# Optimization experiments

Hardware: AMD Instinct MI355X
Metric: run time of the kernel (lower is better)

The kernel has to match this reference:

```python
import jax, jax.numpy as jnp
import numpy as np

HIDDEN = 2048
HEAD_DIM = 256
N_HEADS = 8
N_KV_HEADS = 2
N_GROUPS = N_HEADS // N_KV_HEADS
EPS = 1e-6
WAVELENGTH = 10000.0
ROPE_SCALE = 1.0
NEG_INF = -1e9


def setup_inputs() -> dict:
    key = jax.random.key(0)
    ks = jax.random.split(key, 8)
    B, S = 2, 2048
    hidden_states = jax.random.normal(ks[0], (B, S, HIDDEN), dtype=jnp.float32)
    # additive causal mask: 0 on/below diagonal, -1e9 above
    causal = jnp.tril(jnp.ones((S, S), dtype=bool))
    attention_mask = jnp.where(causal, 0.0, NEG_INF).astype(jnp.float32)[None, None]
    attention_mask = jnp.broadcast_to(attention_mask, (B, 1, S, S))
    sd = 1.0 / np.sqrt(HIDDEN)
    wq = jax.random.normal(ks[1], (HIDDEN, N_HEADS * HEAD_DIM), dtype=jnp.float32) * sd
    wk = jax.random.normal(ks[2], (HIDDEN, N_KV_HEADS * HEAD_DIM), dtype=jnp.float32) * sd
    wv = jax.random.normal(ks[3], (HIDDEN, N_KV_HEADS * HEAD_DIM), dtype=jnp.float32) * sd
    wo = jax.random.normal(ks[4], (N_HEADS * HEAD_DIM, HIDDEN), dtype=jnp.float32) * (1.0 / np.sqrt(N_HEADS * HEAD_DIM))
    q_scale = 1.0 + 0.02 * jax.random.normal(ks[5], (HEAD_DIM,), dtype=jnp.float32)
    k_scale = 1.0 + 0.02 * jax.random.normal(ks[6], (HEAD_DIM,), dtype=jnp.float32)
    return {"hidden_states": hidden_states, "attention_mask": attention_mask,
            "wq": wq, "wk": wk, "wv": wv, "wo": wo,
            "q_scale": q_scale, "k_scale": k_scale}


def _rms_norm(x, scale=None):
    # Gemma3nRMSNorm: compute in float32, optional scale, cast back
    x32 = x.astype(jnp.float32)
    out = x32 * jax.lax.rsqrt(jnp.mean(x32 * x32, axis=-1, keepdims=True) + EPS)
    if scale is not None:
        out = out * scale.astype(jnp.float32)
    return out.astype(x.dtype)


def _rope(x, start_index=0):
    # x: [B, S, H, D]; keras-hub RotaryEmbedding (half-split rotate)
    S, D = x.shape[1], x.shape[-1]
    inv_freq = 1.0 / (WAVELENGTH ** (jnp.arange(0, D, 2, dtype=jnp.float32) / D))
    pos = (jnp.arange(S, dtype=jnp.float32) + start_index) / ROPE_SCALE
    freq = jnp.einsum("s,f->sf", pos, inv_freq)           # [S, D/2]
    emb = jnp.concatenate([freq, freq], axis=-1)          # [S, D]
    cos = jnp.cos(emb)[None, :, None, :].astype(x.dtype)
    sin = jnp.sin(emb)[None, :, None, :].astype(x.dtype)
    x1, x2 = jnp.split(x, 2, axis=-1)
    rot = jnp.concatenate([-x2, x1], axis=-1)
    return x * cos + rot * sin


def reference(hidden_states, attention_mask, wq, wk, wv, wo, q_scale, k_scale):
    B, S, _ = hidden_states.shape
    q = (hidden_states @ wq).reshape(B, S, N_HEADS, HEAD_DIM)
    k = (hidden_states @ wk).reshape(B, S, N_KV_HEADS, HEAD_DIM)
    v = (hidden_states @ wv).reshape(B, S, N_KV_HEADS, HEAD_DIM)
    q = _rope(_rms_norm(q, q_scale))
    k = _rope(_rms_norm(k, k_scale))
    v = _rms_norm(v)  # with_scale=False
    # GQA: repeat KV heads, then BHSD layout
    k = jnp.repeat(k, N_GROUPS, axis=2)
    v = jnp.repeat(v, N_GROUPS, axis=2)
    q = q.transpose(0, 2, 1, 3)
    k = k.transpose(0, 2, 1, 3)
    v = v.transpose(0, 2, 1, 3)
    scores = jnp.einsum("bhqd,bhkd->bhqk", q, k) / np.sqrt(HEAD_DIM)
    scores = scores + attention_mask.astype(scores.dtype)
    probs = jax.nn.softmax(scores.astype(jnp.float32), axis=-1).astype(hidden_states.dtype)
    out = jnp.einsum("bhqk,bhkd->bhqd", probs, v)
    out = out.transpose(0, 2, 1, 3).reshape(B, S, N_HEADS * HEAD_DIM)
    return out @ wo
```

## Files before the change

### kernel.cpp

```cpp
#include <hip/hip_runtime.h>
#include <cstdint>
#include <cstddef>

#define SEQ   2048
#define BATCH 2
#define NH    8
#define NKV   2
#define DH    256
#define HID   2048
#define MR    (BATCH*SEQ)

typedef _Float16 h8 __attribute__((ext_vector_type(8)));
typedef _Float16 h4 __attribute__((ext_vector_type(4)));
typedef float   f32x4 __attribute__((ext_vector_type(4)));

__device__ __forceinline__ f32x4 mfma16(h8 a, h8 b, f32x4 c) {
  return __builtin_amdgcn_mfma_f32_16x16x32_f16(a, b, c, 0, 0, 0);
}
__device__ __forceinline__ void gload16(const void* g, void* l) {
  __builtin_amdgcn_global_load_lds((__attribute__((address_space(1))) void*)g,
                                   (__attribute__((address_space(3))) void*)l,
                                   16, 0, 0);
}

__global__ __launch_bounds__(256) void cvt_f16(const float* __restrict__ in,
                                               _Float16* __restrict__ out, int n4) {
  const int i = blockIdx.x * 256 + threadIdx.x;
  if (i >= n4) return;
  const float4 v = ((const float4*)in)[i];
  h4 o = { (_Float16)v.x, (_Float16)v.y, (_Float16)v.z, (_Float16)v.w };
  ((h4*)out)[i] = o;
}

__global__ __launch_bounds__(256) void wtrans(const float* __restrict__ in,
                                              _Float16* __restrict__ out,
                                              int N, int K) {
  __shared__ float L[32][33];
  const int n0 = blockIdx.x * 32, k0 = blockIdx.y * 32;
  const int t = threadIdx.x;
  const int r = t >> 3, c4 = (t & 7) * 4;
  const float4 v = *(const float4*)&in[(size_t)(k0 + r) * N + n0 + c4];
  L[r][c4] = v.x; L[r][c4 + 1] = v.y; L[r][c4 + 2] = v.z; L[r][c4 + 3] = v.w;
  __syncthreads();
  h4 o = { (_Float16)L[c4][r], (_Float16)L[c4 + 1][r],
           (_Float16)L[c4 + 2][r], (_Float16)L[c4 + 3][r] };
  *(h4*)&out[(size_t)(n0 + r) * K + k0 + c4] = o;
}

__global__ __launch_bounds__(256) void gemm_f16(const _Float16* __restrict__ A,
                                                const _Float16* __restrict__ Bt,
                                                float* __restrict__ C,
                                                const int N, const int K) {
  __shared__ __align__(16) unsigned char sm[32768];
  const int t = threadIdx.x, w = t >> 6, lane = t & 63;
  const int l15 = lane & 15, l4 = lane >> 4;
  const int wr = w >> 1, wc = w & 1;
  const int m0 = blockIdx.y * 128, n0 = blockIdx.x * 128;
  const int swz = (l15 & 7) << 4;
  const size_t rb = (size_t)K * 2;

  int rS[4], cS[4];
#pragma unroll
  for (int i = 0; i < 4; ++i) {
    const int o = i * 4096 + w * 1024 + lane * 16;
    rS[i] = o >> 7;
    cS[i] = (o & 127) ^ ((rS[i] & 7) << 4);
  }
  const char* Ab = (const char*)A + (size_t)m0 * rb;
  const char* Bb = (const char*)Bt + (size_t)n0 * rb;

  f32x4 acc[4][4] = {};

  for (int k0 = 0; k0 < K; k0 += 64) {
    __syncthreads();
#pragma unroll
    for (int i = 0; i < 4; ++i) {
      gload16(Ab + (size_t)rS[i] * rb + k0 * 2 + cS[i], sm + i * 4096 + w * 1024);
      gload16(Bb + (size_t)rS[i] * rb + k0 * 2 + cS[i], sm + 16384 + i * 4096 + w * 1024);
    }
    __syncthreads();
#pragma unroll
    for (int kk = 0; kk < 2; ++kk) {
      const int ko = (kk * 64 + l4 * 16) ^ swz;
      h8 av[4], bv[4];
#pragma unroll
      for (int f = 0; f < 4; ++f) {
        av[f] = *(const h8*)(sm + (wr * 64 + f * 16 + l15) * 128 + ko);
        bv[f] = *(const h8*)(sm + 16384 + (wc * 64 + f * 16 + l15) * 128 + ko);
      }
#pragma unroll
      for (int i = 0; i < 4; ++i)
#pragma unroll
        for (int j = 0; j < 4; ++j)
          acc[i][j] = mfma16(av[i], bv[j], acc[i][j]);
    }
  }
#pragma unroll
  for (int i = 0; i < 4; ++i)
#pragma unroll
    for (int r = 0; r < 4; ++r) {
      const int row = m0 + wr * 64 + i * 16 + l4 * 4 + r;
      float* Cp = C + (size_t)row * N + n0 + wc * 64 + l15;
#pragma unroll
      for (int j = 0; j < 4; ++j) Cp[j * 16] = acc[i][j][r];
    }
}

__global__ __launch_bounds__(256) void norm_rope_q(const float* __restrict__ Qp,
                                                   _Float16* __restrict__ Qh,
                                                   const float* __restrict__ q_scale) {
  const int idx = blockIdx.x;
  const int t = threadIdx.x;
  const int h = idx & 7;
  const int bs = idx >> 3;
  const int s = bs & (SEQ - 1);
  const int b = bs >> 11;
  const float x = Qp[(size_t)bs * 2048 + h * 256 + t];
  float ss = x * x;
#pragma unroll
  for (int off = 32; off; off >>= 1) ss += __shfl_xor(ss, off);
  __shared__ float red[4];
  if ((t & 63) == 0) red[t >> 6] = ss;
  __syncthreads();
  const float tot = red[0] + red[1] + red[2] + red[3];
  const float inv = rsqrtf(tot * (1.0f / 256.0f) + 1e-6f);
  const float xn = x * inv * q_scale[t];
  __shared__ float rowbuf[256];
  rowbuf[t] = xn;
  __syncthreads();
  const int f = t & 127;
  const float invf = expf(-0.07195578415606391f * (float)f);
  float sn, cs;
  sincosf((float)s * invf, &sn, &cs);
  const float other = rowbuf[t ^ 128];
  const float o = (t < 128) ? (xn * cs - other * sn) : (xn * cs + other * sn);
  Qh[((size_t)(b * NH + h) * SEQ + s) * DH + t] = (_Float16)o;
}

__global__ __launch_bounds__(256) void norm_kv(const float* __restrict__ KVp,
                                               _Float16* __restrict__ Kh,
                                               _Float16* __restrict__ Vh,
                                               const float* __restrict__ k_scale) {
  const int idx = blockIdx.x;
  const int t = threadIdx.x;
  const bool isK = idx < 8192;
  const int i = isK ? idx : idx - 8192;
  const int kv = i & 1;
  const int bs = i >> 1;
  const int s = bs & (SEQ - 1);
  const int b = bs >> 11;
  const int col = (isK ? kv * DH : 512 + kv * DH) + t;
  const float x = KVp[(size_t)bs * 1024 + col];
  float ss = x * x;
#pragma unroll
  for (int off = 32; off; off >>= 1) ss += __shfl_xor(ss, off);
  __shared__ float red[4];
  if ((t & 63) == 0) red[t >> 6] = ss;
  __syncthreads();
  const float tot = red[0] + red[1] + red[2] + red[3];
  const float inv = rsqrtf(tot * (1.0f / 256.0f) + 1e-6f);
  float xn = x * inv;
  const size_t o = ((size_t)(b * NKV + kv) * SEQ + s) * DH + t;
  if (isK) {
    xn *= k_scale[t];
    __shared__ float rowbuf[256];
    rowbuf[t] = xn;
    __syncthreads();
    const int f = t & 127;
    const float invf = expf(-0.07195578415606391f * (float)f);
    float sn, cs;
    sincosf((float)s * invf, &sn, &cs);
    const float other = rowbuf[t ^ 128];
    const float ov = (t < 128) ? (xn * cs - other * sn) : (xn * cs + other * sn);
    Kh[o] = (_Float16)ov;
  } else {
    Vh[o] = (_Float16)xn;
  }
}

__global__ __launch_bounds__(256) void transpose_v(const _Float16* __restrict__ Vh,
                                                   _Float16* __restrict__ Vt) {
  __shared__ _Float16 L[32][36];
  const int s0 = blockIdx.x * 32, d0 = blockIdx.y * 32;
  const size_t base = (size_t)blockIdx.z * SEQ * DH;
  const int t = threadIdx.x;
  const int r = t >> 3, c4 = (t & 7) * 4;
  const h4 v = *(const h4*)&Vh[base + (size_t)(s0 + r) * DH + d0 + c4];
  L[r][c4] = v.x; L[r][c4 + 1] = v.y; L[r][c4 + 2] = v.z; L[r][c4 + 3] = v.w;
  __syncthreads();
  h4 o = { L[c4][r], L[c4 + 1][r], L[c4 + 2][r], L[c4 + 3][r] };
  *(h4*)&Vt[base + (size_t)(d0 + r) * SEQ + s0 + c4] = o;
}

__global__ __launch_bounds__(256) void attn_f16(const _Float16* __restrict__ Qh,
                                                const _Float16* __restrict__ Kh,
                                                const _Float16* __restrict__ Vt,
                                                _Float16* __restrict__ Ah) {
  __shared__ __align__(16) unsigned char sm[65536];
  const int pid = blockIdx.x;
  const int h = blockIdx.y, b = blockIdx.z;
  const int kh = h >> 2;
  const int t = threadIdx.x, w = t >> 6, lane = t & 63;
  const int l15 = lane & 15, l4 = lane >> 4;
  const int swz = (l15 & 7) << 4;

  const char* Qg = (const char*)(Qh + (size_t)(b * NH + h) * SEQ * DH);
  const char* Kg = (const char*)(Kh + (size_t)(b * NKV + kh) * SEQ * DH);
  const char* Vg = (const char*)(Vt + (size_t)(b * NKV + kh) * DH * SEQ);

  for (int half = 0; half < 2; ++half) {
    const int qt = (half == 0) ? pid : 31 - pid;
    const int q0 = qt * 64;

    __syncthreads();
#pragma unroll
    for (int i = 0; i < 8; ++i) {
      const int o = i * 4096 + w * 1024 + lane * 16;
      const int row = o >> 9;
      const int off = (o & 511) ^ ((row & 7) << 4);
      gload16(Qg + (size_t)(q0 + row) * 512 + off, sm + i * 4096 + w * 1024);
    }
    __syncthreads();
    h8 qf[8];
    {
      const int qrow = w * 16 + l15;
#pragma unroll
      for (int dc = 0; dc < 8; ++dc)
        qf[dc] = *(const h8*)(sm + qrow * 512 + ((dc * 64 + l4 * 16) ^ swz));
    }
    f32x4 o_acc[16] = {};
    float mrun[4] = { -3e38f, -3e38f, -3e38f, -3e38f };
    float lrun[4] = { 0.f, 0.f, 0.f, 0.f };

    for (int kt = 0; kt <= qt; ++kt) {
      __syncthreads();
#pragma unroll
      for (int i = 0; i < 8; ++i) {
        const int o = i * 4096 + w * 1024 + lane * 16;
        const int row = o >> 9;
        const int off = (o & 511) ^ ((row & 7) << 4);
        gload16(Kg + (size_t)(kt * 64 + row) * 512 + off, sm + i * 4096 + w * 1024);
        const int d = o >> 7;
        const int voff = (o & 127) ^ ((d & 7) << 4);
        gload16(Vg + (size_t)d * (SEQ * 2) + kt * 128 + voff,
                sm + 32768 + i * 4096 + w * 1024);
      }
      __syncthreads();

      f32x4 sc[4];
#pragma unroll
      for (int fk = 0; fk < 4; ++fk) {
        f32x4 z = {};
        sc[fk] = z;
        const int krow = fk * 16 + l15;
#pragma unroll
        for (int dc = 0; dc < 8; ++dc) {
          h8 kf = *(const h8*)(sm + krow * 512 + ((dc * 64 + l4 * 16) ^ swz));
          sc[fk] = mfma16(qf[dc], kf, sc[fk]);
        }
      }

      float p[4][4], alpha[4], mnew[4];
#pragma unroll
      for (int r = 0; r < 4; ++r) {
        const int qg = q0 + w * 16 + l4 * 4 + r;
        float mx = -3e38f;
#pragma unroll
        for (int fk = 0; fk < 4; ++fk) {
          const int kg = kt * 64 + fk * 16 + l15;
          float sv = sc[fk][r] * 0.0625f;
          sv = (kg <= qg) ? sv : -3e38f;
          p[fk][r] = sv;
          mx = fmaxf(mx, sv);
        }
#pragma unroll
        for (int msk = 1; msk < 16; msk <<= 1) mx = fmaxf(mx, __shfl_xor(mx, msk));
        mnew[r] = fmaxf(mrun[r], mx);
        alpha[r] = __expf(mrun[r] - mnew[r]);
        mrun[r] = mnew[r];
        float ls = 0.f;
#pragma unroll
        for (int fk = 0; fk < 4; ++fk) {
          const float e = __expf(p[fk][r] - mnew[r]);
          p[fk][r] = e;
          ls += e;
        }
#pragma unroll
        for (int msk = 1; msk < 16; msk <<= 1) ls += __shfl_xor(ls, msk);
        lrun[r] = lrun[r] * alpha[r] + ls;
      }
#pragma unroll
      for (int fd = 0; fd < 16; ++fd)
#pragma unroll
        for (int r = 0; r < 4; ++r) o_acc[fd][r] *= alpha[r];

      __syncthreads();

      unsigned char* Pb = sm + w * 2048;
#pragma unroll
      for (int fk = 0; fk < 4; ++fk)
#pragma unroll
        for (int r = 0; r < 4; ++r) {
          const int qrow = l4 * 4 + r, k = fk * 16 + l15;
          *(_Float16*)(Pb + qrow * 128 + ((k * 2) ^ ((qrow & 7) << 4))) =
              (_Float16)p[fk][r];
        }
#pragma unroll
      for (int kk = 0; kk < 2; ++kk) {
        const h8 pa = *(const h8*)(Pb + l15 * 128 + ((kk * 64 + l4 * 16) ^ swz));
#pragma unroll
        for (int fd = 0; fd < 16; ++fd) {
          const int d = fd * 16 + l15;
          h8 vf = *(const h8*)(sm + 32768 + d * 128 + ((kk * 64 + l4 * 16) ^ swz));
          o_acc[fd] = mfma16(pa, vf, o_acc[fd]);
        }
      }
    }

#pragma unroll
    for (int r = 0; r < 4; ++r) {
      const float linv = 1.0f / lrun[r];
      const int srow = q0 + w * 16 + l4 * 4 + r;
      _Float16* Op = Ah + (size_t)(b * SEQ + srow) * (NH * DH) + h * DH + l15;
#pragma unroll
      for (int fd = 0; fd < 16; ++fd)
        Op[fd * 16] = (_Float16)(o_acc[fd][r] * linv);
    }
  }
}

extern "C" void kernel_launch(void* const* d_in, const int* in_sizes, int n_in,
                              void* d_out, int out_size, void* d_ws, size_t ws_size,
                              hipStream_t stream) {
  (void)in_sizes; (void)n_in; (void)out_size; (void)ws_size;
  const float* hidden  = (const float*)d_in[0];
  const float* wq      = (const float*)d_in[2];
  const float* wk      = (const float*)d_in[3];
  const float* wv      = (const float*)d_in[4];
  const float* wo      = (const float*)d_in[5];
  const float* q_scale = (const float*)d_in[6];
  const float* k_scale = (const float*)d_in[7];
  float* out = (float*)d_out;

  uint8_t* ws = (uint8_t*)d_ws;
  _Float16* hid_h = (_Float16*)ws;            ws += (size_t)MR * HID * 2;
  _Float16* wq_t  = (_Float16*)ws;            ws += (size_t)HID * HID * 2;
  _Float16* wkv_t = (_Float16*)ws;            ws += (size_t)1024 * HID * 2;
  float*    Qp    = (float*)ws;               ws += (size_t)MR * HID * 4;
  float*    KVp   = (float*)ws;               ws += (size_t)MR * 1024 * 4;
  _Float16* Qh    = (_Float16*)ws;            ws += (size_t)MR * HID * 2;
  _Float16* Kh    = (_Float16*)ws;            ws += (size_t)MR * 512 * 2;
  _Float16* Vh    = (_Float16*)ws;            ws += (size_t)MR * 512 * 2;
  _Float16* Vt    = (_Float16*)ws;            ws += (size_t)MR * 512 * 2;
  _Float16* Ah    = (_Float16*)Qp;

  const dim3 blk(256);
  cvt_f16<<<dim3(8192), blk, 0, stream>>>(hidden, hid_h, MR * HID / 4);
  wtrans<<<dim3(64, 64), blk, 0, stream>>>(wq, wq_t, 2048, 2048);
  wtrans<<<dim3(16, 64), blk, 0, stream>>>(wk, wkv_t, 512, 2048);
  wtrans<<<dim3(16, 64), blk, 0, stream>>>(wv, wkv_t + (size_t)512 * 2048, 512, 2048);
  gemm_f16<<<dim3(16, 32), blk, 0, stream>>>(hid_h, wq_t, Qp, 2048, 2048);
  gemm_f16<<<dim3(8, 32), blk, 0, stream>>>(hid_h, wkv_t, KVp, 1024, 2048);
  wtrans<<<dim3(64, 64), blk, 0, stream>>>(wo, wq_t, 2048, 2048);
  norm_rope_q<<<dim3(32768), blk, 0, stream>>>(Qp, Qh, q_scale);
  norm_kv<<<dim3(16384), blk, 0, stream>>>(KVp, Kh, Vh, k_scale);
  transpose_v<<<dim3(64, 8, 4), blk, 0, stream>>>(Vh, Vt);
  attn_f16<<<dim3(16, 8, 2), blk, 0, stream>>>(Qh, Kh, Vt, Ah);
  gemm_f16<<<dim3(16, 32), blk, 0, stream>>>(Ah, wq_t, out, 2048, 2048);
}
```

Baseline: 420.6 us.

## Fuse QKV projections and keep attention probabilities in registers via shuffles

```diff
diff --git a/kernel.cpp b/kernel.cpp
--- a/kernel.cpp
+++ b/kernel.cpp
@@ -13,6 +13,7 @@
 typedef _Float16 h8 __attribute__((ext_vector_type(8)));
 typedef _Float16 h4 __attribute__((ext_vector_type(4)));
 typedef float   f32x4 __attribute__((ext_vector_type(4)));
+typedef int     i32x4 __attribute__((ext_vector_type(4)));
 
 __device__ __forceinline__ f32x4 mfma16(h8 a, h8 b, f32x4 c) {
   return __builtin_amdgcn_mfma_f32_16x16x32_f16(a, b, c, 0, 0, 0);
@@ -21,6 +22,10 @@
   __builtin_amdgcn_global_load_lds((__attribute__((address_space(1))) void*)g,
                                    (__attribute__((address_space(3))) void*)l,
                                    16, 0, 0);
+}
+__device__ __forceinline__ int pkf16(float a, float b) {
+  auto t = __builtin_amdgcn_cvt_pkrtz(a, b);
+  return __builtin_bit_cast(int, t);
 }
 
 __global__ __launch_bounds__(256) void cvt_f16(const float* __restrict__ in,
@@ -106,7 +111,7 @@
     }
 }
 
-__global__ __launch_bounds__(256) void norm_rope_q(const float* __restrict__ Qp,
+__global__ __launch_bounds__(256) void norm_rope_q(const float* __restrict__ QKVp,
                                                    _Float16* __restrict__ Qh,
                                                    const float* __restrict__ q_scale) {
   const int idx = blockIdx.x;
@@ -115,7 +120,7 @@
   const int bs = idx >> 3;
   const int s = bs & (SEQ - 1);
   const int b = bs >> 11;
-  const float x = Qp[(size_t)bs * 2048 + h * 256 + t];
+  const float x = QKVp[(size_t)bs * 3072 + h * 256 + t];
   float ss = x * x;
 #pragma unroll
   for (int off = 32; off; off >>= 1) ss += __shfl_xor(ss, off);
@@ -134,10 +139,10 @@
   sincosf((float)s * invf, &sn, &cs);
   const float other = rowbuf[t ^ 128];
   const float o = (t < 128) ? (xn * cs - other * sn) : (xn * cs + other * sn);
-  Qh[((size_t)(b * NH + h) * SEQ + s) * DH + t] = (_Float16)o;
-}
-
-__global__ __launch_bounds__(256) void norm_kv(const float* __restrict__ KVp,
+  Qh[((size_t)(b * NH + h) * SEQ + s) * DH + t] = (_Float16)(o * 0.0625f);
+}
+
+__global__ __launch_bounds__(256) void norm_kv(const float* __restrict__ QKVp,
                                                _Float16* __restrict__ Kh,
                                                _Float16* __restrict__ Vh,
                                                const float* __restrict__ k_scale) {
@@ -149,8 +154,8 @@
   const int bs = i >> 1;
   const int s = bs & (SEQ - 1);
   const int b = bs >> 11;
-  const int col = (isK ? kv * DH : 512 + kv * DH) + t;
-  const float x = KVp[(size_t)bs * 1024 + col];
+  const int col = (isK ? 2048 + kv * DH : 2560 + kv * DH) + t;
+  const float x = QKVp[(size_t)bs * 3072 + col];
   float ss = x * x;
 #pragma unroll
   for (int off = 32; off; off >>= 1) ss += __shfl_xor(ss, off);
@@ -192,14 +197,16 @@
   *(h4*)&Vt[base + (size_t)(d0 + r) * SEQ + s0 + c4] = o;
 }
 
-__global__ __launch_bounds__(256) void attn_f16(const _Float16* __restrict__ Qh,
-                                                const _Float16* __restrict__ Kh,
-                                                const _Float16* __restrict__ Vt,
-                                                _Float16* __restrict__ Ah) {
+__global__ __launch_bounds__(256, 2) void attn_f16(const _Float16* __restrict__ Qh,
+                                                   const _Float16* __restrict__ Kh,
+                                                   const _Float16* __restrict__ Vt,
+                                                   _Float16* __restrict__ Ah) {
   __shared__ __align__(16) unsigned char sm[65536];
   const int pid = blockIdx.x;
   const int h = blockIdx.y, b = blockIdx.z;
   const int kh = h >> 2;
+  const int qt = b ? (31 - pid) : pid;
+  const int q0 = qt * 64;
   const int t = threadIdx.x, w = t >> 6, lane = t & 63;
   const int l15 = lane & 15, l4 = lane >> 4;
   const int swz = (l15 & 7) << 4;
@@ -208,124 +215,145 @@
   const char* Kg = (const char*)(Kh + (size_t)(b * NKV + kh) * SEQ * DH);
   const char* Vg = (const char*)(Vt + (size_t)(b * NKV + kh) * DH * SEQ);
 
-  for (int half = 0; half < 2; ++half) {
-    const int qt = (half == 0) ? pid : 31 - pid;
-    const int q0 = qt * 64;
-
+#pragma unroll
+  for (int i = 0; i < 8; ++i) {
+    const int o = i * 4096 + w * 1024 + lane * 16;
+    const int row = o >> 9;
+    const int off = (o & 511) ^ ((row & 7) << 4);
+    gload16(Qg + (size_t)(q0 + row) * 512 + off, sm + i * 4096 + w * 1024);
+  }
+  __syncthreads();
+  h8 qf[8];
+  {
+    const int qrow = w * 16 + l15;
+#pragma unroll
+    for (int dc = 0; dc < 8; ++dc)
+      qf[dc] = *(const h8*)(sm + qrow * 512 + ((dc * 64 + l4 * 16) ^ swz));
+  }
+  f32x4 o_acc[16] = {};
+  float mrun = -3e38f, lrun = 0.f;
+
+  for (int kt = 0; kt <= qt; ++kt) {
     __syncthreads();
 #pragma unroll
     for (int i = 0; i < 8; ++i) {
       const int o = i * 4096 + w * 1024 + lane * 16;
       const int row = o >> 9;
       const int off = (o & 511) ^ ((row & 7) << 4);
-      gload16(Qg + (size_t)(q0 + row) * 512 + off, sm + i * 4096 + w * 1024);
-    }
-    __syncthreads();
-    h8 qf[8];
-    {
-      const int qrow = w * 16 + l15;
-#pragma unroll
-      for (int dc = 0; dc < 8; ++dc)
-        qf[dc] = *(const h8*)(sm + qrow * 512 + ((dc * 64 + l4 * 16) ^ swz));
-    }
-    f32x4 o_acc[16] = {};
-    float mrun[4] = { -3e38f, -3e38f, -3e38f, -3e38f };
-    float lrun[4] = { 0.f, 0.f, 0.f, 0.f };
-
-    for (int kt = 0; kt <= qt; ++kt) {
-      __syncthreads();
-#pragma unroll
-      for (int i = 0; i < 8; ++i) {
-        const int o = i * 4096 + w * 1024 + lane * 16;
-        const int row = o >> 9;
-        const int off = (o & 511) ^ ((row & 7) << 4);
-        gload16(Kg + (size_t)(kt * 64 + row) * 512 + off, sm + i * 4096 + w * 1024);
-        const int d = o >> 7;
-        const int voff = (o & 127) ^ ((d & 7) << 4);
-        gload16(Vg + (size_t)d * (SEQ * 2) + kt * 128 + voff,
-                sm + 32768 + i * 4096 + w * 1024);
+      gload16(Kg + (size_t)(kt * 64 + row) * 512 + off, sm + i * 4096 + w * 1024);
+      const int d = o >> 7;
+      const int voff = (o & 127) ^ ((d & 7) << 4);
+      gload16(Vg + (size_t)d * (SEQ * 2) + kt * 128 + voff,
+              sm + 32768 + i * 4096 + w * 1024);
+    }
+    __syncthreads();
+
+    f32x4 sc[4];
+    __builtin_amdgcn_s_setprio(1);
+#pragma unroll
+    for (int fk = 0; fk < 4; ++fk) {
+      f32x4 z = {};
+      sc[fk] = z;
+      const int krow = fk * 16 + l15;
+#pragma unroll
+      for (int dc = 0; dc < 8; ++dc) {
+        const h8 kf = *(const h8*)(sm + krow * 512 + ((dc * 64 + l4 * 16) ^ swz));
+        sc[fk] = mfma16(kf, qf[dc], sc[fk]);
       }
-      __syncthreads();
-
-      f32x4 sc[4];
-#pragma unroll
-      for (int fk = 0; fk < 4; ++fk) {
-        f32x4 z = {};
-        sc[fk] = z;
-        const int krow = fk * 16 + l15;
-#pragma unroll
-        for (int dc = 0; dc < 8; ++dc) {
-          h8 kf = *(const h8*)(sm + krow * 512 + ((dc * 64 + l4 * 16) ^ swz));
-          sc[fk] = mfma16(qf[dc], kf, sc[fk]);
-        }
+    }
+    __builtin_amdgcn_s_setprio(0);
+
+    float e[4][4];
+    if (kt == qt) {
+#pragma unroll
+      for (int fk = 0; fk < 4; ++fk)
+#pragma unroll
+        for (int r = 0; r < 4; ++r)
+          e[fk][r] = (fk * 16 + l4 * 4 + r <= w * 16 + l15) ? sc[fk][r] : -3e38f;
+    } else {
+#pragma unroll
+      for (int fk = 0; fk < 4; ++fk)
+#pragma unroll
+        for (int r = 0; r < 4; ++r) e[fk][r] = sc[fk][r];
+    }
+    float pm = -3e38f;
+#pragma unroll
+    for (int fk = 0; fk < 4; ++fk)
+#pragma unroll
+      for (int r = 0; r < 4; ++r) pm = fmaxf(pm, e[fk][r]);
+    pm = fmaxf(pm, __shfl_xor(pm, 16));
+    pm = fmaxf(pm, __shfl_xor(pm, 32));
+    const float mnew = fmaxf(mrun, pm);
+    const float alpha = __expf(mrun - mnew);
+    mrun = mnew;
+    float ls = 0.f;
+#pragma unroll
+    for (int fk = 0; fk < 4; ++fk)
+#pragma unroll
+      for (int r = 0; r < 4; ++r) {
+        e[fk][r] = __expf(e[fk][r] - mnew);
+        ls += e[fk][r];
       }
-
-      float p[4][4], alpha[4], mnew[4];
-#pragma unroll
-      for (int r = 0; r < 4; ++r) {
-        const int qg = q0 + w * 16 + l4 * 4 + r;
-        float mx = -3e38f;
-#pragma unroll
-        for (int fk = 0; fk < 4; ++fk) {
-          const int kg = kt * 64 + fk * 16 + l15;
-          float sv = sc[fk][r] * 0.0625f;
-          sv = (kg <= qg) ? sv : -3e38f;
-          p[fk][r] = sv;
-          mx = fmaxf(mx, sv);
-        }
-#pragma unroll
-        for (int msk = 1; msk < 16; msk <<= 1) mx = fmaxf(mx, __shfl_xor(mx, msk));
-        mnew[r] = fmaxf(mrun[r], mx);
-        alpha[r] = __expf(mrun[r] - mnew[r]);
-        mrun[r] = mnew[r];
-        float ls = 0.f;
-#pragma unroll
-        for (int fk = 0; fk < 4; ++fk) {
-          const float e = __expf(p[fk][r] - mnew[r]);
-          p[fk][r] = e;
-          ls += e;
-        }
-#pragma unroll
-        for (int msk = 1; msk < 16; msk <<= 1) ls += __shfl_xor(ls, msk);
-        lrun[r] = lrun[r] * alpha[r] + ls;
+    ls += __shfl_xor(ls, 16);
+    ls += __shfl_xor(ls, 32);
+    lrun = lrun * alpha + ls;
+
+    float al[4];
+#pragma unroll
+    for (int r = 0; r < 4; ++r) al[r] = __shfl(alpha, l4 * 4 + r);
+#pragma unroll
+    for (int fd = 0; fd < 16; ++fd)
+#pragma unroll
+      for (int r = 0; r < 4; ++r) o_acc[fd][r] *= al[r];
+
+    h8 pa[2];
+    const int src0 = l15 + ((l4 & 1) << 5);
+    const int src1 = src0 + 16;
+    const bool lowk = (l4 < 2);
+#pragma unroll
+    for (int kk = 0; kk < 2; ++kk) {
+      const int d0 = pkf16(e[2 * kk][0], e[2 * kk][1]);
+      const int d1 = pkf16(e[2 * kk][2], e[2 * kk][3]);
+      const int d2 = pkf16(e[2 * kk + 1][0], e[2 * kk + 1][1]);
+      const int d3 = pkf16(e[2 * kk + 1][2], e[2 * kk + 1][3]);
+      const int s00 = __shfl(d0, src0);
+      const int s10 = __shfl(d1, src0);
+      const int s20 = __shfl(d2, src0);
+      const int s30 = __shfl(d3, src0);
+      const int s01 = __shfl(d0, src1);
+      const int s11 = __shfl(d1, src1);
+      const int s21 = __shfl(d2, src1);
+      const int s31 = __shfl(d3, src1);
+      const int n0 = lowk ? s00 : s20;
+      const int n1 = lowk ? s10 : s30;
+      const int n2 = lowk ? s01 : s21;
+      const int n3 = lowk ? s11 : s31;
+      i32x4 pw = { n0, n1, n2, n3 };
+      pa[kk] = __builtin_bit_cast(h8, pw);
+    }
+
+    __builtin_amdgcn_s_setprio(1);
+#pragma unroll
+    for (int kk = 0; kk < 2; ++kk) {
+      const int ko = (kk * 64 + l4 * 16) ^ swz;
+#pragma unroll
+      for (int fd = 0; fd < 16; ++fd) {
+        const h8 vf = *(const h8*)(sm + 32768 + (fd * 16 + l15) * 128 + ko);
+        o_acc[fd] = mfma16(pa[kk], vf, o_acc[fd]);
       }
-#pragma unroll
-      for (int fd = 0; fd < 16; ++fd)
-#pragma unroll
-        for (int r = 0; r < 4; ++r) o_acc[fd][r] *= alpha[r];
-
-      __syncthreads();
-
-      unsigned char* Pb = sm + w * 2048;
-#pragma unroll
-      for (int fk = 0; fk < 4; ++fk)
-#pragma unroll
-        for (int r = 0; r < 4; ++r) {
-          const int qrow = l4 * 4 + r, k = fk * 16 + l15;
-          *(_Float16*)(Pb + qrow * 128 + ((k * 2) ^ ((qrow & 7) << 4))) =
-              (_Float16)p[fk][r];
-        }
-#pragma unroll
-      for (int kk = 0; kk < 2; ++kk) {
-        const h8 pa = *(const h8*)(Pb + l15 * 128 + ((kk * 64 + l4 * 16) ^ swz));
-#pragma unroll
-        for (int fd = 0; fd < 16; ++fd) {
-          const int d = fd * 16 + l15;
-          h8 vf = *(const h8*)(sm + 32768 + d * 128 + ((kk * 64 + l4 * 16) ^ swz));
-          o_acc[fd] = mfma16(pa, vf, o_acc[fd]);
-        }
-      }
-    }
-
-#pragma unroll
-    for (int r = 0; r < 4; ++r) {
-      const float linv = 1.0f / lrun[r];
-      const int srow = q0 + w * 16 + l4 * 4 + r;
-      _Float16* Op = Ah + (size_t)(b * SEQ + srow) * (NH * DH) + h * DH + l15;
-#pragma unroll
-      for (int fd = 0; fd < 16; ++fd)
-        Op[fd * 16] = (_Float16)(o_acc[fd][r] * linv);
-    }
+    }
+    __builtin_amdgcn_s_setprio(0);
+  }
+
+  const float inv = 1.0f / lrun;
+#pragma unroll
+  for (int r = 0; r < 4; ++r) {
+    const float linv = __shfl(inv, l4 * 4 + r);
+    const int srow = q0 + w * 16 + l4 * 4 + r;
+    _Float16* Op = Ah + (size_t)(b * SEQ + srow) * (NH * DH) + h * DH + l15;
+#pragma unroll
+    for (int fd = 0; fd < 16; ++fd)
+      Op[fd * 16] = (_Float16)(o_acc[fd][r] * linv);
   }
 }
 
@@ -343,28 +371,25 @@
   float* out = (float*)d_out;
 
   uint8_t* ws = (uint8_t*)d_ws;
-  _Float16* hid_h = (_Float16*)ws;            ws += (size_t)MR * HID * 2;
-  _Float16* wq_t  = (_Float16*)ws;            ws += (size_t)HID * HID * 2;
-  _Float16* wkv_t = (_Float16*)ws;            ws += (size_t)1024 * HID * 2;
-  float*    Qp    = (float*)ws;               ws += (size_t)MR * HID * 4;
-  float*    KVp   = (float*)ws;               ws += (size_t)MR * 1024 * 4;
-  _Float16* Qh    = (_Float16*)ws;            ws += (size_t)MR * HID * 2;
-  _Float16* Kh    = (_Float16*)ws;            ws += (size_t)MR * 512 * 2;
-  _Float16* Vh    = (_Float16*)ws;            ws += (size_t)MR * 512 * 2;
-  _Float16* Vt    = (_Float16*)ws;            ws += (size_t)MR * 512 * 2;
-  _Float16* Ah    = (_Float16*)Qp;
+  _Float16* hid_h = (_Float16*)ws;  ws += (size_t)MR * HID * 2;
+  _Float16* Wt    = (_Float16*)ws;  ws += (size_t)3072 * HID * 2;
+  float*    QKVp  = (float*)ws;     ws += (size_t)MR * 3072 * 4;
+  _Float16* Qh    = (_Float16*)ws;  ws += (size_t)MR * HID * 2;
+  _Float16* Kh    = (_Float16*)ws;  ws += (size_t)MR * 512 * 2;
+  _Float16* Vh    = (_Float16*)ws;  ws += (size_t)MR * 512 * 2;
+  _Float16* Vt    = (_Float16*)ws;  ws += (size_t)MR * 512 * 2;
+  _Float16* Ah    = (_Float16*)QKVp;
 
   const dim3 blk(256);
   cvt_f16<<<dim3(8192), blk, 0, stream>>>(hidden, hid_h, MR * HID / 4);
-  wtrans<<<dim3(64, 64), blk, 0, stream>>>(wq, wq_t, 2048, 2048);
-  wtrans<<<dim3(16, 64), blk, 0, stream>>>(wk, wkv_t, 512, 2048);
-  wtrans<<<dim3(16, 64), blk, 0, stream>>>(wv, wkv_t + (size_t)512 * 2048, 512, 2048);
-  gemm_f16<<<dim3(16, 32), blk, 0, stream>>>(hid_h, wq_t, Qp, 2048, 2048);
-  gemm_f16<<<dim3(8, 32), blk, 0, stream>>>(hid_h, wkv_t, KVp, 1024, 2048);
-  wtrans<<<dim3(64, 64), blk, 0, stream>>>(wo, wq_t, 2048, 2048);
-  norm_rope_q<<<dim3(32768), blk, 0, stream>>>(Qp, Qh, q_scale);
-  norm_kv<<<dim3(16384), blk, 0, stream>>>(KVp, Kh, Vh, k_scale);
+  wtrans<<<dim3(64, 64), blk, 0, stream>>>(wq, Wt, 2048, 2048);
+  wtrans<<<dim3(16, 64), blk, 0, stream>>>(wk, Wt + (size_t)2048 * 2048, 512, 2048);
+  wtrans<<<dim3(16, 64), blk, 0, stream>>>(wv, Wt + (size_t)2560 * 2048, 512, 2048);
+  gemm_f16<<<dim3(24, 32), blk, 0, stream>>>(hid_h, Wt, QKVp, 3072, 2048);
+  wtrans<<<dim3(64, 64), blk, 0, stream>>>(wo, Wt, 2048, 2048);
+  norm_rope_q<<<dim3(32768), blk, 0, stream>>>(QKVp, Qh, q_scale);
+  norm_kv<<<dim3(16384), blk, 0, stream>>>(QKVp, Kh, Vh, k_scale);
   transpose_v<<<dim3(64, 8, 4), blk, 0, stream>>>(Vh, Vt);
-  attn_f16<<<dim3(16, 8, 2), blk, 0, stream>>>(Qh, Kh, Vt, Ah);
-  gemm_f16<<<dim3(16, 32), blk, 0, stream>>>(Ah, wq_t, out, 2048, 2048);
-}
+  attn_f16<<<dim3(32, 8, 2), blk, 0, stream>>>(Qh, Kh, Vt, Ah);
+  gemm_f16<<<dim3(16, 32), blk, 0, stream>>>(Ah, Wt, out, 2048, 2048);
+}
```

Measured after the change: 395.0 us. 1.06x faster.
